# Kernel optimization log

Measured on AMD Instinct MI355X. Metric: run time of the kernel, lower is better.

Reference implementation:

```python
import jax, jax.numpy as jnp
import numpy as np

N = 50000   # num_nodes
R = 32      # num_relations
D_IN = 128
D_HID = 128
E = 600000  # num_edges
T = 8192    # num scored triplets


def setup_inputs() -> dict:
    key = jax.random.key(0)
    ks = jax.random.split(key, 10)
    return {
        "x_emb": jax.random.normal(ks[0], (N, D_IN), jnp.float32),
        "W": jax.random.normal(ks[1], (R, D_IN, D_HID), jnp.float32) * 0.05,
        "W_root": jax.random.normal(ks[2], (D_IN, D_HID), jnp.float32) * 0.05,
        "bias": jnp.zeros((D_HID,), jnp.float32),
        "rel_emb": jax.random.normal(ks[3], (R, D_HID), jnp.float32),
        "edge_index": jax.random.randint(ks[4], (2, E), 0, N, jnp.int64),
        "edge_type": jax.random.randint(ks[5], (E,), 0, R, jnp.int64),
        "head_idx": jax.random.randint(ks[6], (T,), 0, N, jnp.int64),
        "tail_idx": jax.random.randint(ks[7], (T,), 0, N, jnp.int64),
        "rel_idx": jax.random.randint(ks[8], (T,), 0, R, jnp.int64),
    }


def reference(x_emb, W, W_root, bias, rel_emb,
              edge_index, edge_type, head_idx, tail_idx, rel_idx):
    # --- RGCNConv (PyG semantics: per-relation mean aggregation + root + bias) ---
    src, tgt = edge_index[0], edge_index[1]
    # segment id combining target node and relation: mean is computed per (node, relation)
    seg = tgt * R + edge_type                              # [E]
    ones = jnp.ones((seg.shape[0],), x_emb.dtype)
    cnt = jax.ops.segment_sum(ones, seg, num_segments=N * R)   # [N*R]
    norm = 1.0 / jnp.maximum(cnt[seg], 1.0)                    # [E]
    # Aggregate source features first (W is linear, so transform after aggregation)
    agg = jax.ops.segment_sum(x_emb[src] * norm[:, None], seg, num_segments=N * R)
    agg = agg.reshape(N, R, D_IN)                              # [N, R, d_in]
    h = jnp.einsum('nri,rio->no', agg, W) + x_emb @ W_root + bias  # [N, d_hid]
    h = jax.nn.relu(h)
    # --- DistMult triplet scoring: sum(h * r * t) ---
    scores = jnp.sum(h[head_idx] * rel_emb[rel_idx] * h[tail_idx], axis=-1)  # [T]
    return scores
```

## Files before the change

### kernel.cpp

```cpp
#include <hip/hip_runtime.h>
#include <hip/hip_bf16.h>

typedef unsigned int u32;
typedef unsigned short u16;
typedef short short8 __attribute__((ext_vector_type(8)));
typedef float f32x4 __attribute__((ext_vector_type(4)));

#define R_ 32
#define KEYS_PER_B 2048
#define SORT_STRIDE 1024
#define CAP 16
#define MAXU 16384
#define NSPLIT 4
#define NRG 8

static __device__ __forceinline__ u16 f2bf(float f) {
  u32 u = __float_as_uint(f);
  u = (u + 0x7FFFu + ((u >> 16) & 1u)) >> 16;
  return (u16)u;
}
static __device__ __forceinline__ u32 pk2(float a, float b) {
  __hip_bfloat162 h2 = __float22bfloat162_rn(make_float2(a, b));
  union { __hip_bfloat162 h; u32 u; } cv; cv.h = h2; return cv.u;
}

static __device__ __forceinline__ int sort_key(int ct, int r) {
  return (ct >> 6) * KEYS_PER_B + ((ct >> 4) & 3) * 512 + r * 16 + (ct & 15);
}

__global__ __launch_bounds__(256) void k_prep(
    const float* __restrict__ x, const float* __restrict__ W,
    const float* __restrict__ Wroot, u16* __restrict__ xb,
    u16* __restrict__ wp, u16* __restrict__ wrootp,
    const int* __restrict__ head, const int* __restrict__ tail,
    int* __restrict__ map, int* __restrict__ inv, int* __restrict__ cnt,
    int* __restrict__ hist, int n4, int convNB, int histZB, int T) {
  __shared__ u32 lds[8192];
  int bx = blockIdx.x;
  const int t = threadIdx.x;
  if (bx < convNB) {
    int i = bx * 256 + t;
    if (i >= n4) return;
    const float4 f = ((const float4*)x)[i];
    u32 lo = (u32)f2bf(f.x) | ((u32)f2bf(f.y) << 16);
    u32 hi = (u32)f2bf(f.z) | ((u32)f2bf(f.w) << 16);
    ((uint2*)xb)[i] = make_uint2(lo, hi);
    return;
  }
  bx -= convNB;
  if (bx < 33) {
    const int rr = bx;
    const float* src = (rr < 32) ? (W + (size_t)rr * (128 * 128)) : Wroot;
#pragma unroll
    for (int k = 0; k < 16; ++k) {
      const int fi = k * 256 + t;
      const float4 f = ((const float4*)src)[fi];
      u32 lo = (u32)f2bf(f.x) | ((u32)f2bf(f.y) << 16);
      u32 hi = (u32)f2bf(f.z) | ((u32)f2bf(f.w) << 16);
      ((uint2*)lds)[fi] = make_uint2(lo, hi);
    }
    __syncthreads();
    const u16* l16 = (const u16*)lds;
#pragma unroll
    for (int p = 0; p < 8; ++p) {
      const int v = p * 256 + t;
      const int lane = v & 63, ks = (v >> 6) & 3, ct = v >> 8;
      const int i0 = ks * 32 + (lane >> 4) * 8;
      const int o  = ct * 16 + (lane & 15);
      u32 w01 = (u32)l16[(i0 + 0) * 128 + o] | ((u32)l16[(i0 + 1) * 128 + o] << 16);
      u32 w23 = (u32)l16[(i0 + 2) * 128 + o] | ((u32)l16[(i0 + 3) * 128 + o] << 16);
      u32 w45 = (u32)l16[(i0 + 4) * 128 + o] | ((u32)l16[(i0 + 5) * 128 + o] << 16);
      u32 w67 = (u32)l16[(i0 + 6) * 128 + o] | ((u32)l16[(i0 + 7) * 128 + o] << 16);
      u16* dst = (rr < 32) ? (wp + ((size_t)((rr * 8 + ct) * 4 + ks) * 64 + lane) * 8)
                           : (wrootp + ((size_t)((ct * 4 + ks) * 64 + lane)) * 8);
      *(uint4*)dst = make_uint4(w01, w23, w45, w67);
    }
    return;
  }
  bx -= 33;
  if (bx < histZB) {
    ((int4*)hist)[bx * 256 + t] = make_int4(0, 0, 0, 0);
    return;
  }
  bx -= histZB;
  int i = bx * 256 + t;
  if (i >= 2 * T) return;
  int n = (i < T) ? head[i] : tail[i - T];
  if (atomicCAS(map + n, -1, -2) == -1) {
    int c = atomicAdd(cnt, 1) + 1;
    inv[c] = n;
    map[n] = c;
  }
}

__global__ void k_hist(const int* __restrict__ ei, const int* __restrict__ et,
                       const int* __restrict__ map, int* __restrict__ hist, int E) {
  int e = blockIdx.x * 256 + threadIdx.x;
  if (e >= E) return;
  int mt = map[ei[E + e]];
  if (mt >= 0) atomicAdd(hist + sort_key(mt, et[e]), 1);
}

__global__ __launch_bounds__(256) void k_scan_local(const int* __restrict__ hist,
                                                    int* __restrict__ offs) {
  __shared__ int wsum[4];
  int b = blockIdx.x, t = threadIdx.x;
  size_t base = (size_t)b * KEYS_PER_B + (size_t)t * 8;
  int4 a = *(const int4*)(hist + base);
  int4 c = *(const int4*)(hist + base + 4);
  int v[8] = {a.x, a.y, a.z, a.w, c.x, c.y, c.z, c.w};
  int s = 0;
#pragma unroll
  for (int i = 0; i < 8; ++i) s += v[i];
  int lane = t & 63, w = t >> 6;
  int x = s;
#pragma unroll
  for (int off = 1; off < 64; off <<= 1) {
    int y = __shfl_up(x, off);
    if (lane >= off) x += y;
  }
  if (lane == 63) wsum[w] = x;
  __syncthreads();
  int wb = 0;
  for (int i = 0; i < w; ++i) wb += wsum[i];
  int ex = wb + x - s;
  int o[8];
#pragma unroll
  for (int i = 0; i < 8; ++i) { o[i] = ex; ex += v[i]; }
  *(int4*)(offs + base) = make_int4(o[0], o[1], o[2], o[3]);
  *(int4*)(offs + base + 4) = make_int4(o[4], o[5], o[6], o[7]);
}

__global__ void k_scatter(const int* __restrict__ ei, const int* __restrict__ et,
                          const int* __restrict__ map,
                          int* __restrict__ offs, u32* __restrict__ sorted, int E) {
  int e = blockIdx.x * 256 + threadIdx.x;
  if (e >= E) return;
  int mt = map[ei[E + e]];
  if (mt < 0) return;
  int src = ei[e];
  int p = atomicAdd(offs + sort_key(mt, et[e]), 1);
  if (p < SORT_STRIDE)
    sorted[(size_t)(mt >> 6) * SORT_STRIDE + p] = (u32)src | ((u32)(mt & 63) << 16);
}

#define PHASE(RR, RI, XV, EVB)                                                 \
  {                                                                            \
    const int r = (RR);                                                        \
    const int Er = __builtin_amdgcn_readlane(eAll, r);                         \
    _Pragma("unroll") for (int rr = 0; rr < 16; ++rr)                          \
        *(u32*)(aggb + (size_t)(w * 16 + rr) * 136 + 2 * lane) = 0;            \
    {                                                                          \
      const int nB = min(Er - sCur, CAP);                                      \
      int curRow = -1, rc = 0;                                                 \
      float v0 = 0.f, v1 = 0.f;                                                \
      _Pragma("unroll") for (int j = 0; j < CAP; ++j) {                        \
        if (j < nB) {                                                          \
          int e = __builtin_amdgcn_readlane((int)(EVB), j);                    \
          int tl = (e >> 16) & 63;                                             \
          if (tl != curRow) {                                                  \
            if (rc > 0) {                                                      \
              float sc = __builtin_amdgcn_rcpf((float)rc);                     \
              *(u32*)(aggb + (size_t)curRow * 136 + 2 * lane) =                \
                  pk2(v0 * sc, v1 * sc);                                       \
            }                                                                  \
            curRow = tl; v0 = 0.f; v1 = 0.f; rc = 0;                           \
          }                                                                    \
          v0 += __uint_as_float((XV)[j] << 16);                                \
          v1 += __uint_as_float((XV)[j] & 0xFFFF0000u);                        \
          ++rc;                                                                \
        }                                                                      \
      }                                                                        \
      for (int p = sCur + CAP; p < Er; ++p) {                                  \
        u32 e = srt[p];                                                        \
        u32 xvv = *(const u32*)(xb + (size_t)(e & 0xFFFFu) * 128 + 2 * lane);  \
        int tl = (int)((e >> 16) & 63);                                        \
        if (tl != curRow) {                                                    \
          if (rc > 0) {                                                        \
            float sc = __builtin_amdgcn_rcpf((float)rc);                       \
            *(u32*)(aggb + (size_t)curRow * 136 + 2 * lane) =                  \
                pk2(v0 * sc, v1 * sc);                                         \
          }                                                                    \
          curRow = tl; v0 = 0.f; v1 = 0.f; rc = 0;                             \
        }                                                                      \
        v0 += __uint_as_float(xvv << 16);                                      \
        v1 += __uint_as_float(xvv & 0xFFFF0000u);                              \
        ++rc;                                                                  \
      }                                                                        \
      if (rc > 0) {                                                            \
        float sc = __builtin_amdgcn_rcpf((float)rc);                           \
        *(u32*)(aggb + (size_t)curRow * 136 + 2 * lane) =                      \
            pk2(v0 * sc, v1 * sc);                                             \
      }                                                                        \
    }                                                                          \
    asm volatile("s_waitcnt lgkmcnt(0)" ::: "memory");                         \
    __builtin_amdgcn_sched_barrier(0);                                         \
    __builtin_amdgcn_s_barrier();                                              \
    __builtin_amdgcn_sched_barrier(0);                                         \
    short8 bfr[4][2];                                                          \
    _Pragma("unroll") for (int ks = 0; ks < 4; ++ks)                           \
      _Pragma("unroll") for (int c = 0; c < 2; ++c)                            \
        bfr[ks][c] = *(const short8*)(wp +                                     \
            ((size_t)(((r * 8 + wct0 + c) * 4 + ks) * 64 + lane)) * 8);        \
    __builtin_amdgcn_sched_barrier(0);                                         \
    if ((RI) + 2 < NRG) {                                                      \
      const int sN = __builtin_amdgcn_readlane(eAll, r + 1);                   \
      const int eN = __builtin_amdgcn_readlane(eAll, r + 2);                   \
      (EVB) = ev2;                                                             \
      const int nBn = min(eN - sN, CAP);                                       \
      _Pragma("unroll") for (int j = 0; j < CAP; ++j) {                        \
        if (j < nBn) {                                                         \
          int e = __builtin_amdgcn_readlane((int)(EVB), j);                    \
          (XV)[j] = *(const u32*)(xb + (size_t)(e & 0xFFFF) * 128 + 2 * lane); \
        }                                                                      \
      }                                                                        \
      if ((RI) + 3 < NRG) {                                                    \
        int pcn = eN + m;                                                      \
        if (pcn > clampP) pcn = clampP;                                        \
        ev2 = srt[pcn];                                                        \
      }                                                                        \
    }                                                                          \
    _Pragma("unroll") for (int ks = 0; ks < 4; ++ks) {                         \
      const int kb = ks * 32 + q * 8;                                          \
      short8 af[4];                                                            \
      _Pragma("unroll") for (int rt = 0; rt < 4; ++rt)                         \
        af[rt] = *(const short8*)(aggb + (size_t)(rt * 16 + m) * 136 + kb);    \
      _Pragma("unroll") for (int c = 0; c < 2; ++c)                            \
        _Pragma("unroll") for (int rt = 0; rt < 4; ++rt)                       \
          acc[rt][c] = __builtin_amdgcn_mfma_f32_16x16x32_bf16(                \
              af[rt], bfr[ks][c], acc[rt][c], 0, 0, 0);                        \
    }                                                                          \
    asm volatile("s_waitcnt lgkmcnt(0)" ::: "memory");                         \
    __builtin_amdgcn_sched_barrier(0);                                         \
    __builtin_amdgcn_s_barrier();                                              \
    __builtin_amdgcn_sched_barrier(0);                                         \
    sCur = Er;                                                                 \
  }

__global__ __launch_bounds__(256) void k_batch(
    const u16* __restrict__ xb, const u16* __restrict__ wp, const u16* __restrict__ wrootp,
    const float* __restrict__ bias, const u32* __restrict__ sorted,
    const int* __restrict__ offs, const int* __restrict__ inv,
    const int* __restrict__ cnt, float* __restrict__ h) {
  __shared__ u16 aggb[64 * 136];
  const int nUsed = cnt[0] + 1;
  const int qs = blockIdx.x & (NSPLIT - 1);
  const int b = blockIdx.x >> 2;
  const int t = threadIdx.x;
  const int nb = b * 64;
  if (nb >= nUsed) return;
  const int r0 = qs * NRG;
  const int lane = t & 63, w = t >> 6;
  const int m = lane & 15, q = lane >> 4;
  const int keyBase = b * KEYS_PER_B;
  const int wkBase = keyBase + w * 512;
  const u32* srt = sorted + (size_t)b * SORT_STRIDE;

  const int nEdge = offs[keyBase + KEYS_PER_B - 1];
  const int clampP = (nEdge > 0) ? nEdge - 1 : 0;
  const int eAll = offs[wkBase + (lane & 31) * 16 + 15];
  int sCur = (w == 0 && qs == 0) ? 0 : offs[wkBase + r0 * 16 - 1];

  const int E0 = __builtin_amdgcn_readlane(eAll, r0);
  const int E1 = __builtin_amdgcn_readlane(eAll, r0 + 1);

  u32 evBufA, evBufB, ev2;
  u32 xvA[CAP], xvB[CAP];
  {
    int pc = sCur + m;
    if (pc > clampP) pc = clampP;
    evBufA = srt[pc];
  }
  {
    const int nB = min(E0 - sCur, CAP);
#pragma unroll
    for (int j = 0; j < CAP; ++j) {
      if (j < nB) {
        int e = __builtin_amdgcn_readlane((int)evBufA, j);
        xvA[j] = *(const u32*)(xb + (size_t)(e & 0xFFFF) * 128 + 2 * lane);
      }
    }
  }
  {
    int pc = E0 + m;
    if (pc > clampP) pc = clampP;
    evBufB = srt[pc];
  }
  {
    const int nB = min(E1 - E0, CAP);
#pragma unroll
    for (int j = 0; j < CAP; ++j) {
      if (j < nB) {
        int e = __builtin_amdgcn_readlane((int)evBufB, j);
        xvB[j] = *(const u32*)(xb + (size_t)(e & 0xFFFF) * 128 + 2 * lane);
      }
    }
  }
  {
    int pc = E1 + m;
    if (pc > clampP) pc = clampP;
    ev2 = srt[pc];
  }

  const short8 zero8 = {0, 0, 0, 0, 0, 0, 0, 0};
  f32x4 acc[4][2];
#pragma unroll
  for (int rt = 0; rt < 4; ++rt)
#pragma unroll
    for (int c = 0; c < 2; ++c) acc[rt][c] = (f32x4){0.f, 0.f, 0.f, 0.f};
  const int wct0 = w * 2;

  if (qs == 0) {
    int nodeR[4]; bool vR[4];
#pragma unroll
    for (int rt = 0; rt < 4; ++rt) {
      int crow = nb + rt * 16 + m;
      vR[rt] = crow < nUsed;
      nodeR[rt] = inv[vR[rt] ? crow : (nUsed - 1)];
    }
#pragma unroll
    for (int ks = 0; ks < 4; ++ks) {
      const int kb = ks * 32 + q * 8;
      short8 af[4];
#pragma unroll
      for (int rt = 0; rt < 4; ++rt)
        af[rt] = vR[rt] ? *(const short8*)(xb + (size_t)nodeR[rt] * 128 + kb) : zero8;
#pragma unroll
      for (int c = 0; c < 2; ++c) {
        short8 bf = *(const short8*)(wrootp + ((size_t)(((wct0 + c) * 4 + ks) * 64 + lane)) * 8);
#pragma unroll
        for (int rt = 0; rt < 4; ++rt)
          acc[rt][c] = __builtin_amdgcn_mfma_f32_16x16x32_bf16(af[rt], bf, acc[rt][c], 0, 0, 0);
      }
    }
  }

  for (int ri = 0; ri < NRG; ri += 2) {
    PHASE(r0 + ri, ri, xvA, evBufA)
    PHASE(r0 + ri + 1, ri + 1, xvB, evBufB)
  }

  float* hq = h + (size_t)qs * MAXU * 128;
#pragma unroll
  for (int c = 0; c < 2; ++c) {
    const int col = (wct0 + c) * 16 + m;
    const float bv = (qs == 0) ? bias[col] : 0.f;
#pragma unroll
    for (int rt = 0; rt < 4; ++rt) {
#pragma unroll
      for (int g = 0; g < 4; ++g) {
        const int row = nb + rt * 16 + q * 4 + g;
        if (row < nUsed) hq[(size_t)row * 128 + col] = acc[rt][c][g] + bv;
      }
    }
  }
}

__global__ void k_score(const float* __restrict__ h, const float* __restrict__ rel_emb,
                        const int* __restrict__ map,
                        const int* __restrict__ head, const int* __restrict__ tail,
                        const int* __restrict__ rel, float* __restrict__ out, int T) {
  int lane = threadIdx.x & 63, w = threadIdx.x >> 6;
  int gid = blockIdx.x * 4 + w;
  if (gid >= T) return;
  const int hr = map[head[gid]];
  const int tr = map[tail[gid]];
  const size_t ho = (size_t)hr * 128 + 2 * lane;
  const size_t to = (size_t)tr * 128 + 2 * lane;
  float hx = 0.f, hy = 0.f, tx = 0.f, ty = 0.f;
#pragma unroll
  for (int s = 0; s < NSPLIT; ++s) {
    const float2 a = *(const float2*)(h + (size_t)s * (MAXU * 128) + ho);
    const float2 c = *(const float2*)(h + (size_t)s * (MAXU * 128) + to);
    hx += a.x; hy += a.y; tx += c.x; ty += c.y;
  }
  hx = hx > 0.f ? hx : 0.f;
  hy = hy > 0.f ? hy : 0.f;
  tx = tx > 0.f ? tx : 0.f;
  ty = ty > 0.f ? ty : 0.f;
  const float2 r2 = *(const float2*)(rel_emb + (size_t)rel[gid] * 128 + 2 * lane);
  float s = hx * r2.x * tx + hy * r2.y * ty;
#pragma unroll
  for (int off = 32; off > 0; off >>= 1) s += __shfl_down(s, off);
  if (lane == 0) out[gid] = s;
}

extern "C" void kernel_launch(void* const* d_in, const int* in_sizes, int n_in,
                              void* d_out, int out_size, void* d_ws, size_t ws_size,
                              hipStream_t stream) {
  const float* x     = (const float*)d_in[0];
  const float* W     = (const float*)d_in[1];
  const float* Wroot = (const float*)d_in[2];
  const float* bias  = (const float*)d_in[3];
  const float* relE  = (const float*)d_in[4];
  const int* ei      = (const int*)d_in[5];
  const int* et      = (const int*)d_in[6];
  const int* headI   = (const int*)d_in[7];
  const int* tailI   = (const int*)d_in[8];
  const int* relI    = (const int*)d_in[9];
  float* out = (float*)d_out;

  const int N = in_sizes[0] / 128;
  const int E = in_sizes[6];
  const int T = in_sizes[7];
  const int NB2 = MAXU / 64;
  const int NKEYS2 = NB2 * KEYS_PER_B;

  char* p = (char*)d_ws;
  auto alloc = [&](size_t bytes) -> void* {
    void* r = (void*)p;
    p += (bytes + 255) & ~(size_t)255;
    return r;
  };
  u16* xb     = (u16*)alloc((size_t)N * 128 * 2);
  u16* wp     = (u16*)alloc((size_t)32 * 2048 * 8 * 2);
  u16* wrootp = (u16*)alloc((size_t)2048 * 8 * 2);
  int* hist   = (int*)alloc((size_t)NKEYS2 * 4);
  int* map    = (int*)alloc((size_t)(N + 64) * 4);
  int* cnt    = map + N;
  int* inv    = (int*)alloc((size_t)MAXU * 4);
  int* offs   = (int*)alloc((size_t)NKEYS2 * 4);
  u32* sorted = (u32*)alloc((size_t)NB2 * SORT_STRIDE * 4);
  float* h    = (float*)alloc((size_t)NSPLIT * MAXU * 128 * 4);

  const int n4 = N * 128 / 4;
  const int convNB = (n4 + 255) / 256;
  const int histZB = NKEYS2 / 1024;
  const int markNB = (2 * T + 255) / 256;

  hipMemsetAsync(map, 0xFF, (size_t)(N + 64) * 4, stream);
  k_prep<<<convNB + 33 + histZB + markNB, 256, 0, stream>>>(
      x, W, Wroot, xb, wp, wrootp, headI, tailI, map, inv, cnt, hist,
      n4, convNB, histZB, T);
  k_hist<<<(E + 255) / 256, 256, 0, stream>>>(ei, et, map, hist, E);
  k_scan_local<<<NB2, 256, 0, stream>>>(hist, offs);
  k_scatter<<<(E + 255) / 256, 256, 0, stream>>>(ei, et, map, offs, sorted, E);
  k_batch<<<NB2 * NSPLIT, 256, 0, stream>>>(xb, wp, wrootp, bias, sorted, offs, inv, cnt, h);
  k_score<<<(T + 3) / 4, 256, 0, stream>>>(h, relE, map, headI, tailI, relI, out, T);
}
```

Before: 188.8 us.

## Replace global histogram/scan/scatter sort with per-block binning and in-LDS counting sort

Replaces the three-pass global edge sort (histogram, scan, scatter over a large key array) with a single binning pass that appends packed edges (source, local row, relation) into per-64-node bins using one atomic counter per bin. Each k_batch block then does its own counting sort in shared memory over its bin, filtered to its relation quarter, and reads edges from LDS. This removes two kernel launches and the large hist/offs arrays along with their zeroing. The cost is redundant bin reads across the NSPLIT blocks and extra LDS atomics. CAP is also lowered from 16 to 12. Source indices are masked to 16 bits, which assumes N fits in 65536.

```diff
diff --git a/kernel.cpp b/kernel.cpp
--- a/kernel.cpp
+++ b/kernel.cpp
@@ -7,9 +7,8 @@
 typedef float f32x4 __attribute__((ext_vector_type(4)));
 
 #define R_ 32
-#define KEYS_PER_B 2048
 #define SORT_STRIDE 1024
-#define CAP 16
+#define CAP 12
 #define MAXU 16384
 #define NSPLIT 4
 #define NRG 8
@@ -22,10 +21,6 @@
 static __device__ __forceinline__ u32 pk2(float a, float b) {
   __hip_bfloat162 h2 = __float22bfloat162_rn(make_float2(a, b));
   union { __hip_bfloat162 h; u32 u; } cv; cv.h = h2; return cv.u;
-}
-
-static __device__ __forceinline__ int sort_key(int ct, int r) {
-  return (ct >> 6) * KEYS_PER_B + ((ct >> 4) & 3) * 512 + r * 16 + (ct & 15);
 }
 
 __global__ __launch_bounds__(256) void k_prep(
@@ -34,7 +29,7 @@
     u16* __restrict__ wp, u16* __restrict__ wrootp,
     const int* __restrict__ head, const int* __restrict__ tail,
     int* __restrict__ map, int* __restrict__ inv, int* __restrict__ cnt,
-    int* __restrict__ hist, int n4, int convNB, int histZB, int T) {
+    int n4, int convNB, int T) {
   __shared__ u32 lds[8192];
   int bx = blockIdx.x;
   const int t = threadIdx.x;
@@ -78,11 +73,6 @@
     return;
   }
   bx -= 33;
-  if (bx < histZB) {
-    ((int4*)hist)[bx * 256 + t] = make_int4(0, 0, 0, 0);
-    return;
-  }
-  bx -= histZB;
   int i = bx * 256 + t;
   if (i >= 2 * T) return;
   int n = (i < T) ? head[i] : tail[i - T];
@@ -93,61 +83,23 @@
   }
 }
 
-__global__ void k_hist(const int* __restrict__ ei, const int* __restrict__ et,
-                       const int* __restrict__ map, int* __restrict__ hist, int E) {
-  int e = blockIdx.x * 256 + threadIdx.x;
-  if (e >= E) return;
-  int mt = map[ei[E + e]];
-  if (mt >= 0) atomicAdd(hist + sort_key(mt, et[e]), 1);
-}
-
-__global__ __launch_bounds__(256) void k_scan_local(const int* __restrict__ hist,
-                                                    int* __restrict__ offs) {
-  __shared__ int wsum[4];
-  int b = blockIdx.x, t = threadIdx.x;
-  size_t base = (size_t)b * KEYS_PER_B + (size_t)t * 8;
-  int4 a = *(const int4*)(hist + base);
-  int4 c = *(const int4*)(hist + base + 4);
-  int v[8] = {a.x, a.y, a.z, a.w, c.x, c.y, c.z, c.w};
-  int s = 0;
-#pragma unroll
-  for (int i = 0; i < 8; ++i) s += v[i];
-  int lane = t & 63, w = t >> 6;
-  int x = s;
-#pragma unroll
-  for (int off = 1; off < 64; off <<= 1) {
-    int y = __shfl_up(x, off);
-    if (lane >= off) x += y;
-  }
-  if (lane == 63) wsum[w] = x;
-  __syncthreads();
-  int wb = 0;
-  for (int i = 0; i < w; ++i) wb += wsum[i];
-  int ex = wb + x - s;
-  int o[8];
-#pragma unroll
-  for (int i = 0; i < 8; ++i) { o[i] = ex; ex += v[i]; }
-  *(int4*)(offs + base) = make_int4(o[0], o[1], o[2], o[3]);
-  *(int4*)(offs + base + 4) = make_int4(o[4], o[5], o[6], o[7]);
-}
-
-__global__ void k_scatter(const int* __restrict__ ei, const int* __restrict__ et,
-                          const int* __restrict__ map,
-                          int* __restrict__ offs, u32* __restrict__ sorted, int E) {
+__global__ void k_bin(const int* __restrict__ ei, const int* __restrict__ et,
+                      const int* __restrict__ map,
+                      int* __restrict__ bcnt, u32* __restrict__ bins, int E) {
   int e = blockIdx.x * 256 + threadIdx.x;
   if (e >= E) return;
   int mt = map[ei[E + e]];
   if (mt < 0) return;
-  int src = ei[e];
-  int p = atomicAdd(offs + sort_key(mt, et[e]), 1);
+  int p = atomicAdd(bcnt + (mt >> 6), 1) + 1;
   if (p < SORT_STRIDE)
-    sorted[(size_t)(mt >> 6) * SORT_STRIDE + p] = (u32)src | ((u32)(mt & 63) << 16);
+    bins[(size_t)(mt >> 6) * SORT_STRIDE + p] =
+        ((u32)ei[e] & 0xFFFFu) | ((u32)(mt & 63) << 16) | ((u32)et[e] << 22);
 }
 
 #define PHASE(RR, RI, XV, EVB)                                                 \
   {                                                                            \
     const int r = (RR);                                                        \
-    const int Er = __builtin_amdgcn_readlane(eAll, r);                         \
+    const int Er = __builtin_amdgcn_readlane(eAll, (RI));                      \
     _Pragma("unroll") for (int rr = 0; rr < 16; ++rr)                          \
         *(u32*)(aggb + (size_t)(w * 16 + rr) * 136 + 2 * lane) = 0;            \
     {                                                                          \
@@ -172,7 +124,7 @@
         }                                                                      \
       }                                                                        \
       for (int p = sCur + CAP; p < Er; ++p) {                                  \
-        u32 e = srt[p];                                                        \
+        u32 e = sortedL[p];                                                    \
         u32 xvv = *(const u32*)(xb + (size_t)(e & 0xFFFFu) * 128 + 2 * lane);  \
         int tl = (int)((e >> 16) & 63);                                        \
         if (tl != curRow) {                                                    \
@@ -204,8 +156,8 @@
             ((size_t)(((r * 8 + wct0 + c) * 4 + ks) * 64 + lane)) * 8);        \
     __builtin_amdgcn_sched_barrier(0);                                         \
     if ((RI) + 2 < NRG) {                                                      \
-      const int sN = __builtin_amdgcn_readlane(eAll, r + 1);                   \
-      const int eN = __builtin_amdgcn_readlane(eAll, r + 2);                   \
+      const int sN = __builtin_amdgcn_readlane(eAll, (RI) + 1);                \
+      const int eN = __builtin_amdgcn_readlane(eAll, (RI) + 2);                \
       (EVB) = ev2;                                                             \
       const int nBn = min(eN - sN, CAP);                                       \
       _Pragma("unroll") for (int j = 0; j < CAP; ++j) {                        \
@@ -215,9 +167,9 @@
         }                                                                      \
       }                                                                        \
       if ((RI) + 3 < NRG) {                                                    \
-        int pcn = eN + m;                                                      \
+        int pcn = eN + lane;                                                   \
         if (pcn > clampP) pcn = clampP;                                        \
-        ev2 = srt[pcn];                                                        \
+        ev2 = sortedL[pcn];                                                    \
       }                                                                        \
     }                                                                          \
     _Pragma("unroll") for (int ks = 0; ks < 4; ++ks) {                         \
@@ -239,10 +191,13 @@
 
 __global__ __launch_bounds__(256) void k_batch(
     const u16* __restrict__ xb, const u16* __restrict__ wp, const u16* __restrict__ wrootp,
-    const float* __restrict__ bias, const u32* __restrict__ sorted,
-    const int* __restrict__ offs, const int* __restrict__ inv,
+    const float* __restrict__ bias, const u32* __restrict__ bins,
+    const int* __restrict__ bcnt, const int* __restrict__ inv,
     const int* __restrict__ cnt, float* __restrict__ h) {
   __shared__ u16 aggb[64 * 136];
+  __shared__ u32 sortedL[SORT_STRIDE];
+  __shared__ int offsL[512];
+  __shared__ int wsum[4];
   const int nUsed = cnt[0] + 1;
   const int qs = blockIdx.x & (NSPLIT - 1);
   const int b = blockIdx.x >> 2;
@@ -252,24 +207,59 @@
   const int r0 = qs * NRG;
   const int lane = t & 63, w = t >> 6;
   const int m = lane & 15, q = lane >> 4;
-  const int keyBase = b * KEYS_PER_B;
-  const int wkBase = keyBase + w * 512;
-  const u32* srt = sorted + (size_t)b * SORT_STRIDE;
-
-  const int nEdge = offs[keyBase + KEYS_PER_B - 1];
-  const int clampP = (nEdge > 0) ? nEdge - 1 : 0;
-  const int eAll = offs[wkBase + (lane & 31) * 16 + 15];
-  int sCur = (w == 0 && qs == 0) ? 0 : offs[wkBase + r0 * 16 - 1];
-
-  const int E0 = __builtin_amdgcn_readlane(eAll, r0);
-  const int E1 = __builtin_amdgcn_readlane(eAll, r0 + 1);
+  const int wct0 = w * 2;
+
+  const int nTile = min(bcnt[b] + 1, SORT_STRIDE);
+  const u32* binB = bins + (size_t)b * SORT_STRIDE;
+  offsL[t] = 0; offsL[256 + t] = 0;
+  __syncthreads();
+  for (int i = t; i < nTile; i += 256) {
+    u32 v = binB[i];
+    if ((int)(v >> 25) == qs)
+      atomicAdd(&offsL[(((v >> 20) & 3) << 7) + (((v >> 22) & 7) << 4) + ((v >> 16) & 15)], 1);
+  }
+  __syncthreads();
+  {
+    int h0 = offsL[2 * t], h1 = offsL[2 * t + 1];
+    int s = h0 + h1;
+    int x = s;
+#pragma unroll
+    for (int off = 1; off < 64; off <<= 1) {
+      int y = __shfl_up(x, off);
+      if (lane >= off) x += y;
+    }
+    if (lane == 63) wsum[w] = x;
+    __syncthreads();
+    int wb = 0;
+    for (int i = 0; i < w; ++i) wb += wsum[i];
+    int ex = wb + x - s;
+    offsL[2 * t] = ex;
+    offsL[2 * t + 1] = ex + h0;
+  }
+  __syncthreads();
+  for (int i = t; i < nTile; i += 256) {
+    u32 v = binB[i];
+    if ((int)(v >> 25) == qs) {
+      int pos = atomicAdd(&offsL[(((v >> 20) & 3) << 7) + (((v >> 22) & 7) << 4) + ((v >> 16) & 15)], 1);
+      sortedL[pos] = v;
+    }
+  }
+  __syncthreads();
+
+  const int nG = offsL[511];
+  const int clampP = (nG > 0) ? nG - 1 : 0;
+  const int eAll = offsL[(w << 7) + ((lane & 7) << 4) + 15];
+  int sCur = (w == 0) ? 0 : offsL[(w << 7) - 1];
+
+  const int E0 = __builtin_amdgcn_readlane(eAll, 0);
+  const int E1 = __builtin_amdgcn_readlane(eAll, 1);
 
   u32 evBufA, evBufB, ev2;
   u32 xvA[CAP], xvB[CAP];
   {
-    int pc = sCur + m;
+    int pc = sCur + lane;
     if (pc > clampP) pc = clampP;
-    evBufA = srt[pc];
+    evBufA = sortedL[pc];
   }
   {
     const int nB = min(E0 - sCur, CAP);
@@ -282,9 +272,9 @@
     }
   }
   {
-    int pc = E0 + m;
+    int pc = E0 + lane;
     if (pc > clampP) pc = clampP;
-    evBufB = srt[pc];
+    evBufB = sortedL[pc];
   }
   {
     const int nB = min(E1 - E0, CAP);
@@ -297,9 +287,9 @@
     }
   }
   {
-    int pc = E1 + m;
+    int pc = E1 + lane;
     if (pc > clampP) pc = clampP;
-    ev2 = srt[pc];
+    ev2 = sortedL[pc];
   }
 
   const short8 zero8 = {0, 0, 0, 0, 0, 0, 0, 0};
@@ -308,7 +298,6 @@
   for (int rt = 0; rt < 4; ++rt)
 #pragma unroll
     for (int c = 0; c < 2; ++c) acc[rt][c] = (f32x4){0.f, 0.f, 0.f, 0.f};
-  const int wct0 = w * 2;
 
   if (qs == 0) {
     int nodeR[4]; bool vR[4];
@@ -404,7 +393,6 @@
   const int E = in_sizes[6];
   const int T = in_sizes[7];
   const int NB2 = MAXU / 64;
-  const int NKEYS2 = NB2 * KEYS_PER_B;
 
   char* p = (char*)d_ws;
   auto alloc = [&](size_t bytes) -> void* {
@@ -415,26 +403,21 @@
   u16* xb     = (u16*)alloc((size_t)N * 128 * 2);
   u16* wp     = (u16*)alloc((size_t)32 * 2048 * 8 * 2);
   u16* wrootp = (u16*)alloc((size_t)2048 * 8 * 2);
-  int* hist   = (int*)alloc((size_t)NKEYS2 * 4);
-  int* map    = (int*)alloc((size_t)(N + 64) * 4);
+  int* map    = (int*)alloc((size_t)(N + 64 + NB2) * 4);
   int* cnt    = map + N;
+  int* bcnt   = map + N + 64;
   int* inv    = (int*)alloc((size_t)MAXU * 4);
-  int* offs   = (int*)alloc((size_t)NKEYS2 * 4);
-  u32* sorted = (u32*)alloc((size_t)NB2 * SORT_STRIDE * 4);
+  u32* bins   = (u32*)alloc((size_t)NB2 * SORT_STRIDE * 4);
   float* h    = (float*)alloc((size_t)NSPLIT * MAXU * 128 * 4);
 
   const int n4 = N * 128 / 4;
   const int convNB = (n4 + 255) / 256;
-  const int histZB = NKEYS2 / 1024;
   const int markNB = (2 * T + 255) / 256;
 
-  hipMemsetAsync(map, 0xFF, (size_t)(N + 64) * 4, stream);
-  k_prep<<<convNB + 33 + histZB + markNB, 256, 0, stream>>>(
-      x, W, Wroot, xb, wp, wrootp, headI, tailI, map, inv, cnt, hist,
-      n4, convNB, histZB, T);
-  k_hist<<<(E + 255) / 256, 256, 0, stream>>>(ei, et, map, hist, E);
-  k_scan_local<<<NB2, 256, 0, stream>>>(hist, offs);
-  k_scatter<<<(E + 255) / 256, 256, 0, stream>>>(ei, et, map, offs, sorted, E);
-  k_batch<<<NB2 * NSPLIT, 256, 0, stream>>>(xb, wp, wrootp, bias, sorted, offs, inv, cnt, h);
+  hipMemsetAsync(map, 0xFF, (size_t)(N + 64 + NB2) * 4, stream);
+  k_prep<<<convNB + 33 + markNB, 256, 0, stream>>>(
+      x, W, Wroot, xb, wp, wrootp, headI, tailI, map, inv, cnt, n4, convNB, T);
+  k_bin<<<(E + 255) / 256, 256, 0, stream>>>(ei, et, map, bcnt, bins, E);
+  k_batch<<<NB2 * NSPLIT, 256, 0, stream>>>(xb, wp, wrootp, bias, bins, bcnt, inv, cnt, h);
   k_score<<<(T + 3) / 4, 256, 0, stream>>>(h, relE, map, headI, tailI, relI, out, T);
 }
```

Measured after the change: 302.6 us. 60.3% more time.
